# Performance work log

Hardware: AMD Instinct MI355X
Metric: run time of the kernel (lower is better)

The kernel has to match this reference:

```python
import jax, jax.numpy as jnp
from jax import lax
import numpy as np

K = 256   # kernel_size == hidden channels (Haar basis size)
S = 16    # stride
BN_EPS = 1e-5


def _haar_matrix_unnorm(n):
    if n == 2:
        return np.array([[1.0, 1.0], [1.0, -1.0]])
    prev = _haar_matrix_unnorm(n // 2)
    top = np.kron(prev, np.array([1.0, 1.0]))
    bot = np.kron(np.eye(n // 2), np.array([1.0, -1.0]))
    return np.concatenate((top, bot))


def haar_matrix(n):
    h = _haar_matrix_unnorm(n)
    return h / np.linalg.norm(h, axis=1, keepdims=True)


def setup_inputs() -> dict:
    key = jax.random.key(0)
    ks = jax.random.split(key, 8)
    B, T = 64, 32768
    haar = jnp.asarray(haar_matrix(K), dtype=jnp.float32)          # [K, K]
    x = jax.random.normal(ks[0], (B, 1, T), dtype=jnp.float32)
    return {
        "x": x,
        # BitwiseConv1d(1, K, K, stride=S, padding=K)
        "conv_w": haar[:, None, :],                                 # [K, 1, K] (OIH)
        "conv_b": 0.01 * jax.random.normal(ks[1], (K,), dtype=jnp.float32),
        "conv_gate": jax.random.uniform(ks[2], (K, 1, K), dtype=jnp.float32),
        "conv_scale": jnp.ones((K,), dtype=jnp.float32),            # adaptive per-out-channel scale
        # BatchNorm1d(K)
        "bn_gamma": jnp.ones((K,), dtype=jnp.float32),
        "bn_beta": jnp.zeros((K,), dtype=jnp.float32),
        # BitwiseConvTranspose1d(K, 1, K, stride=S)
        "ct_w": haar.T[:, None, :],                                 # [K(in), 1(out), K] (IOH, torch layout)
        "ct_b": 0.01 * jax.random.normal(ks[3], (1,), dtype=jnp.float32),
        "ct_gate": jax.random.uniform(ks[4], (K, 1, K), dtype=jnp.float32),
        "ct_scale": jnp.ones((1,), dtype=jnp.float32),
    }


def _forward(x, conv_w, conv_b, conv_gate, conv_scale, bn_gamma, bn_beta,
             ct_w, ct_b, ct_gate, ct_scale):
    T = x.shape[2]
    # --- BitwiseConv1d: gated weights (in_bin/weight_bin = identity) ---
    # gate binarization maps gate -> (gate + 1) / 2, multiplied into weights
    w = conv_w * (conv_gate + 1.0) * 0.5                            # [K,1,K]
    h = lax.conv_general_dilated(
        x, w, window_strides=(S,), padding=[(K, K)],
        dimension_numbers=("NCH", "OIH", "NCH"))                  # [B,K,L]
    h = conv_scale[None, :, None] * (h + conv_b[None, :, None])    # adaptive scaling
    # --- ReLU then BatchNorm1d (training-mode batch statistics) ---
    h = jax.nn.relu(h)
    mu = jnp.mean(h, axis=(0, 2), keepdims=True)
    var = jnp.mean((h - mu) ** 2, axis=(0, 2), keepdims=True)
    h = (h - mu) * lax.rsqrt(var + BN_EPS)
    h = h * bn_gamma[None, :, None] + bn_beta[None, :, None]
    # --- BitwiseConvTranspose1d: gated weights, expressed as dilated conv ---
    wt = ct_w * (ct_gate + 1.0) * 0.5                               # [K_in, 1, K]
    # torch IOH -> regular-conv OIH with kernel flipped
    wr = jnp.flip(jnp.transpose(wt, (1, 0, 2)), axis=-1)            # [1, K, K]
    y = lax.conv_general_dilated(
        h, wr, window_strides=(1,), padding=[(K - 1, K - 1)],
        lhs_dilation=(S,), dimension_numbers=("NCH", "OIH", "NCH"))
    y = ct_scale[None, :, None] * (y + ct_b[None, :, None])
    # crop: out[:, :, K : T + K]
    return y[:, :, K:T + K]


def reference(x, conv_w, conv_b, conv_gate, conv_scale, bn_gamma, bn_beta,
              ct_w, ct_b, ct_gate, ct_scale):
    return _forward(x, conv_w, conv_b, conv_gate, conv_scale, bn_gamma, bn_beta,
                    ct_w, ct_b, ct_gate, ct_scale)
```

## Files before the change

kernel.cpp:

```cpp
#include <hip/hip_runtime.h>
#include <hip/hip_bf16.h>

#define BB 64
#define TT 32768
#define KK 256
#define LL 2065
#define LT1 64
#define NLT1 33
#define NP1 (BB*NLT1)
#define NJ 19
#define NPT3 8

typedef __attribute__((ext_vector_type(8))) short short8;
typedef __attribute__((ext_vector_type(4))) float f32x4;
typedef __attribute__((ext_vector_type(4))) int int4v;
typedef __attribute__((ext_vector_type(2))) unsigned int uint2v;

__device__ __forceinline__ unsigned short f2bf(float f) {
    unsigned u = __builtin_bit_cast(unsigned, f);
    unsigned r = (u + 0x7FFFu + ((u >> 16) & 1u)) >> 16;
    return (unsigned short)r;
}
__device__ __forceinline__ unsigned pkbf(float a, float b) {
    unsigned r;
    asm("v_cvt_pk_bf16_f32 %0, %1, %2" : "=v"(r) : "v"(a), "v"(b));
    return r;
}
__device__ __forceinline__ float bf2f(unsigned short v) {
    return __builtin_bit_cast(float, (unsigned)v << 16);
}
__device__ __forceinline__ void gload_lds16(const void* g, void* l) {
    __builtin_amdgcn_global_load_lds(
        (const __attribute__((address_space(1))) unsigned int*)g,
        (__attribute__((address_space(3))) unsigned int*)l, 16, 0, 0);
}
__device__ __forceinline__ int slot_pi(int s) {
    int gg = s >> 4, f = s & 15;
    if (f < 8)  return 128 + 8*gg + f;
    if (f < 12) return 64 + 4*gg + (f - 8);
    if (f < 14) return 32 + 2*gg + (f - 12);
    if (f == 14) return 16 + gg;
    return gg;
}

__global__ void k0s_wpf(const float* __restrict__ cw, const float* __restrict__ cgt,
                        const float* __restrict__ cs, const float* __restrict__ cb,
                        float* __restrict__ Wpf, float* __restrict__ cbsp)
{
    int idx = blockIdx.x*256 + threadIdx.x;
    if (idx < 2304) {
        int g = idx / 144, e = idx - g*144;
        int lvl = e >> 4, m = e & 15;
        int j = 16*g + m;
        int o;
        switch (lvl) {
            case 0: o = 0; break;
            case 1: o = 1; break;
            case 2: o = 2 + (g>>3); break;
            case 3: o = 4 + (g>>2); break;
            case 4: o = 8 + (g>>1); break;
            case 5: o = 16 + g; break;
            case 6: o = 32 + 2*g + (m>>3); break;
            case 7: o = 64 + 4*g + (m>>2); break;
            default: o = 128 + 8*g + (m>>1); break;
        }
        Wpf[idx] = cs[o] * cw[o*KK + j] * (cgt[o*KK + j] + 1.0f) * 0.5f;
    }
    if (blockIdx.x == 0) {
        int s = threadIdx.x;
        int o = slot_pi(s);
        cbsp[s] = cs[o]*cb[o];
    }
}

__global__ __launch_bounds__(256, 2)
void k1_conv(const float* __restrict__ x, const float* __restrict__ Wpf,
             const float* __restrict__ cbsp,
             unsigned short* __restrict__ hout,
             float* __restrict__ psum, float* __restrict__ psq)
{
    __shared__ __align__(16) float xs[80*20];
    __shared__ __align__(16) unsigned short hb[64*256];
    __shared__ float redS[8*256];
    __shared__ float redQ[8*256];

    const int tid   = threadIdx.x;
    const int ltile = blockIdx.x;
    const int b     = blockIdx.y;
    const int l0    = ltile * LT1;
    const int lane  = tid & 63;
    const int w     = tid >> 6;
    const int gp    = lane & 15;
    const int cg    = lane >> 4;

    {
        const float* xb = x + (size_t)b*TT;
        const long pos0 = (long)l0*16 - 256;
        #pragma unroll
        for (int i = 0; i < 5; ++i) {
            int it = tid + i*256;
            long p = pos0 + it;
            xs[(it>>4)*20 + (it&15)] = (p >= 0 && p < TT) ? xb[p] : 0.0f;
        }
    }

    float wv[144];
    {
        const f32x4* wsrc = (const f32x4*)(Wpf + gp*144);
        #pragma unroll
        for (int i = 0; i < 36; ++i) {
            f32x4 t = wsrc[i];
            wv[4*i] = t[0]; wv[4*i+1] = t[1]; wv[4*i+2] = t[2]; wv[4*i+3] = t[3];
        }
    }
    f32x4 cbf[4];
    #pragma unroll
    for (int i = 0; i < 4; ++i) cbf[i] = *(const f32x4*)(cbsp + gp*16 + 4*i);

    const int wrow = (gp & 1) ? (8 + (gp >> 1))
                              : ((4056416 >> (3*(gp >> 1))) & 7);
    const float cbcoarse = cbsp[16*wrow + 15];
    __syncthreads();

    #pragma unroll 1
    for (int it = 0; it < 4; ++it) {
        const int col = w*16 + it*4 + cg;
        float xr[16];
        {
            const f32x4* xp = (const f32x4*)&xs[(col + gp)*20];
            #pragma unroll
            for (int i = 0; i < 4; ++i) {
                f32x4 t = xp[i];
                xr[4*i] = t[0]; xr[4*i+1] = t[1]; xr[4*i+2] = t[2]; xr[4*i+3] = t[3];
            }
        }
        float p0 = 0.f, p1 = 0.f, p2 = 0.f, p3 = 0.f, p4 = 0.f;
        #pragma unroll
        for (int m = 0; m < 16; ++m) {
            p0 = fmaf(wv[m],      xr[m], p0);
            p1 = fmaf(wv[16 + m], xr[m], p1);
            p2 = fmaf(wv[32 + m], xr[m], p2);
            p3 = fmaf(wv[48 + m], xr[m], p3);
            p4 = fmaf(wv[64 + m], xr[m], p4);
        }
        p4 += __shfl_xor(p4, 1);
        p3 += __shfl_xor(p3, 1); p3 += __shfl_xor(p3, 2);
        p2 += __shfl_xor(p2, 1); p2 += __shfl_xor(p2, 2); p2 += __shfl_xor(p2, 4);
        p1 += __shfl_xor(p1, 1); p1 += __shfl_xor(p1, 2); p1 += __shfl_xor(p1, 4);
        p1 += __shfl_xor(p1, 8);
        p0 += __shfl_xor(p0, 1); p0 += __shfl_xor(p0, 2); p0 += __shfl_xor(p0, 4);
        p0 += __shfl_xor(p0, 8);

        float v8[8], v7[4], v6[2], v5 = 0.f;
        #pragma unroll
        for (int k = 0; k < 8; ++k)
            v8[k] = fmaf(wv[128 + 2*k + 1], xr[2*k + 1], wv[128 + 2*k]*xr[2*k]);
        #pragma unroll
        for (int k = 0; k < 4; ++k) {
            float a = wv[112 + 4*k]*xr[4*k];
            a = fmaf(wv[112 + 4*k + 1], xr[4*k + 1], a);
            a = fmaf(wv[112 + 4*k + 2], xr[4*k + 2], a);
            v7[k] = fmaf(wv[112 + 4*k + 3], xr[4*k + 3], a);
        }
        #pragma unroll
        for (int k = 0; k < 2; ++k) {
            float a = 0.f;
            #pragma unroll
            for (int m = 0; m < 8; ++m) a = fmaf(wv[96 + 8*k + m], xr[8*k + m], a);
            v6[k] = a;
        }
        #pragma unroll
        for (int m = 0; m < 16; ++m) v5 = fmaf(wv[80 + m], xr[m], v5);

        const int swz = col & 7;
        unsigned short* hcol = hb + col*256;
        {
            float h0 = fmaxf(v8[0] + cbf[0][0], 0.f), h1 = fmaxf(v8[1] + cbf[0][1], 0.f);
            float h2 = fmaxf(v8[2] + cbf[0][2], 0.f), h3 = fmaxf(v8[3] + cbf[0][3], 0.f);
            float h4 = fmaxf(v8[4] + cbf[1][0], 0.f), h5 = fmaxf(v8[5] + cbf[1][1], 0.f);
            float h6 = fmaxf(v8[6] + cbf[1][2], 0.f), h7 = fmaxf(v8[7] + cbf[1][3], 0.f);
            int4v pk = { (int)pkbf(h0,h1), (int)pkbf(h2,h3),
                         (int)pkbf(h4,h5), (int)pkbf(h6,h7) };
            *(int4v*)(hcol + (((2*gp) ^ swz) << 3)) = pk;
        }
        {
            unsigned short* c1 = hcol + (((2*gp + 1) ^ swz) << 3);
            float h0 = fmaxf(v7[0] + cbf[2][0], 0.f), h1 = fmaxf(v7[1] + cbf[2][1], 0.f);
            float h2 = fmaxf(v7[2] + cbf[2][2], 0.f), h3 = fmaxf(v7[3] + cbf[2][3], 0.f);
            uint2v pk2 = { pkbf(h0,h1), pkbf(h2,h3) };
            *(uint2v*)c1 = pk2;
            float h4 = fmaxf(v6[0] + cbf[3][0], 0.f), h5 = fmaxf(v6[1] + cbf[3][1], 0.f);
            *(unsigned*)(c1 + 4) = pkbf(h4, h5);
            float h6 = fmaxf(v5 + cbf[3][2], 0.f);
            c1[6] = (unsigned short)(pkbf(h6, h6) & 0xffffu);
        }
        {
            float pc;
            if (gp & 1) pc = p4;
            else pc = (wrow == 0) ? p0 : (wrow == 1) ? p1
                     : (wrow <= 3) ? p2 : p3;
            float hc = fmaxf(pc + cbcoarse, 0.f);
            unsigned short* cc = hcol + (((2*wrow + 1) ^ swz) << 3);
            cc[7] = (unsigned short)(pkbf(hc, hc) & 0xffffu);
        }
    }
    __syncthreads();

    float s8[8], q8[8];
    #pragma unroll
    for (int j = 0; j < 8; ++j) { s8[j] = 0.f; q8[j] = 0.f; }
    const int chunk = tid & 31;
    const int colb  = tid >> 5;
    #pragma unroll
    for (int k = 0; k < 8; ++k) {
        int col = colb + k*8;
        int l = l0 + col;
        if (l < LL) {
            int4v v = *(const int4v*)(hb + col*256 + ((chunk ^ (col & 7)) << 3));
            *(int4v*)(hout + (((size_t)(b*LL + l)) << 8) + chunk*8) = v;
            #pragma unroll
            for (int i = 0; i < 4; ++i) {
                unsigned uu = (unsigned)v[i];
                float f0 = bf2f((unsigned short)(uu & 0xffffu));
                float f1 = bf2f((unsigned short)(uu >> 16));
                s8[2*i] += f0;   q8[2*i]   = fmaf(f0, f0, q8[2*i]);
                s8[2*i+1] += f1; q8[2*i+1] = fmaf(f1, f1, q8[2*i+1]);
            }
        }
    }
    {
        f32x4 a0 = { s8[0], s8[1], s8[2], s8[3] }, a1 = { s8[4], s8[5], s8[6], s8[7] };
        f32x4 b0 = { q8[0], q8[1], q8[2], q8[3] }, b1 = { q8[4], q8[5], q8[6], q8[7] };
        *(f32x4*)&redS[colb*256 + chunk*8]     = a0;
        *(f32x4*)&redS[colb*256 + chunk*8 + 4] = a1;
        *(f32x4*)&redQ[colb*256 + chunk*8]     = b0;
        *(f32x4*)&redQ[colb*256 + chunk*8 + 4] = b1;
    }
    __syncthreads();
    {
        float s = 0.f, q = 0.f;
        #pragma unroll
        for (int k = 0; k < 8; ++k) {
            s += redS[k*256 + tid];
            q += redQ[k*256 + tid];
        }
        size_t base = ((size_t)(b*NLT1 + ltile)) << 8;
        psum[base + tid] = s;
        psq [base + tid] = q;
    }
}

__global__ __launch_bounds__(256)
void k2_bn(const float* __restrict__ psum, const float* __restrict__ psq,
           const float* __restrict__ bng, const float* __restrict__ bnb,
           const float* __restrict__ ctw, const float* __restrict__ ctg,
           const float* __restrict__ ctscale,
           float* __restrict__ W3s, float* __restrict__ SWS)
{
    __shared__ double rs[4], rq[4];
    __shared__ float s_a, s_bc;
    __shared__ float swl[256];
    const int c = blockIdx.x;
    const int tid = threadIdx.x;
    const int o = slot_pi(c);
    double s = 0.0, q = 0.0;
    for (int i = tid; i < NP1; i += 256) {
        s += (double)psum[((size_t)i << 8) + c];
        q += (double)psq [((size_t)i << 8) + c];
    }
    for (int off = 32; off > 0; off >>= 1) {
        s += __shfl_down(s, off);
        q += __shfl_down(q, off);
    }
    if ((tid & 63) == 0) { rs[tid >> 6] = s; rq[tid >> 6] = q; }
    __syncthreads();
    if (tid == 0) {
        double st = rs[0]+rs[1]+rs[2]+rs[3];
        double qt = rq[0]+rq[1]+rq[2]+rq[3];
        const double cnt = (double)BB * (double)LL;
        double mu = st / cnt;
        double var = qt / cnt - mu*mu;
        float rsig = (float)(1.0 / sqrt(var + 1e-5));
        float a = bng[o] * rsig;
        s_a = a;
        s_bc = bnb[o] - (float)mu * a;
    }
    __syncthreads();
    float a = s_a, bc = s_bc, scl = ctscale[0];
    int gi = o*KK + tid;
    float wt = ctw[gi] * (ctg[gi] + 1.0f) * 0.5f;
    W3s[tid*KK + c] = scl * a * wt;
    swl[tid] = wt * bc;
    __syncthreads();
    if (tid < 16) {
        float acc2 = 0.0f;
        #pragma unroll
        for (int d = 0; d < 16; ++d) acc2 += swl[d*16 + tid];
        SWS[c*16 + tid] = acc2;
    }
}

__global__ __launch_bounds__(256)
void k2b_const(const float* __restrict__ SWS, const float* __restrict__ ctb,
               const float* __restrict__ ctscale, float* __restrict__ C2)
{
    __shared__ float accb[16][17];
    int tid = threadIdx.x;
    int r = tid & 15, cc = tid >> 4;
    float s = 0.0f;
    #pragma unroll
    for (int i = 0; i < 16; ++i) s += SWS[(cc*16 + i)*16 + r];
    accb[cc][r] = s;
    __syncthreads();
    if (tid < 16) {
        float t = 0.0f;
        #pragma unroll
        for (int i = 0; i < 16; ++i) t += accb[i][tid];
        C2[tid] = ctscale[0] * (t + ctb[0]);
    }
}

__global__ void k2c_b2f(const float* __restrict__ W3s, unsigned short* __restrict__ B2f)
{
    int idx = blockIdx.x*256 + threadIdx.x;
    int lane = idx & 63;
    int ntG  = (idx>>6) & 3;
    int kk   = (idx>>8) & 7;
    int j    = idx>>11;
    int c    = kk*32 + ((lane>>4)<<3);
    int r    = lane & 15;
    int d    = ntG + 15 - j;
    short8 v;
    if (d >= 0 && d <= 15) {
        const float* wr = W3s + (size_t)(16*d + r)*KK + c;
        #pragma unroll
        for (int i = 0; i < 8; ++i) v[i] = (short)f2bf(wr[i]);
    } else {
        #pragma unroll
        for (int i = 0; i < 8; ++i) v[i] = 0;
    }
    *(short8*)(B2f + (size_t)idx*8) = v;
}

__global__ __launch_bounds__(512, 1)
void k3_synth(const unsigned short* __restrict__ h, const unsigned short* __restrict__ B2f,
              const float* __restrict__ C2, float* __restrict__ out)
{
    __shared__ __align__(16) char As[272*512];
    const int tid  = threadIdx.x;
    const int lane = tid & 63;
    const int w    = tid >> 6;
    const int b    = blockIdx.y;
    const int P0   = blockIdx.x * 64;

    const char* hbase = (const char*)h + (((size_t)(b*LL) + 4*P0 + 1) << 9);

    {
        const int rl = lane >> 5;
        #pragma unroll
        for (int i = 0; i < 17; ++i) {
            int r0  = w*34 + i*2;
            int row = r0 + rl;
            int chunk = (lane & 31) ^ ((row >> 2) & 7);
            gload_lds16(hbase + (size_t)row*512 + chunk*16, As + r0*512);
        }
    }
    __syncthreads();

    const int li = lane & 15;
    const int gq = lane >> 4;

    f32x4 acc[4][4];
    #pragma unroll
    for (int mt = 0; mt < 4; ++mt)
        #pragma unroll
        for (int nt = 0; nt < 4; ++nt) acc[mt][nt] = (f32x4){0.f,0.f,0.f,0.f};

    #pragma unroll 1
    for (int jj = 0; jj < 3; ++jj) {
        const int j = w + jj*8;
        if (j >= NJ) break;
        short8 bfA[4], bfB[4];
        #pragma unroll
        for (int nt = 0; nt < 4; ++nt)
            bfA[nt] = *(const short8*)(B2f + (((size_t)(j*8 + 0)*4 + nt)*64 + lane)*8);
        #pragma unroll
        for (int kk = 0; kk < 8; ++kk) {
            if (kk < 7) {
                #pragma unroll
                for (int nt = 0; nt < 4; ++nt)
                    bfB[nt] = *(const short8*)(B2f + (((size_t)(j*8 + kk+1)*4 + nt)*64 + lane)*8);
            }
            short8 af[4];
            #pragma unroll
            for (int mt = 0; mt < 4; ++mt) {
                int row = 64*mt + 4*li + j;
                int p = (kk*4 + gq) ^ ((row >> 2) & 7);
                af[mt] = *(const short8*)(As + row*512 + p*16);
            }
            __builtin_amdgcn_s_setprio(1);
            #pragma unroll
            for (int mt = 0; mt < 4; ++mt)
                #pragma unroll
                for (int nt = 0; nt < 4; ++nt)
                    acc[mt][nt] = __builtin_amdgcn_mfma_f32_16x16x32_bf16(af[mt], bfA[nt], acc[mt][nt], 0, 0, 0);
            __builtin_amdgcn_s_setprio(0);
            #pragma unroll
            for (int nt = 0; nt < 4; ++nt) bfA[nt] = bfB[nt];
        }
    }
    __syncthreads();

    float* red = (float*)As;
    #pragma unroll
    for (int mt = 0; mt < 4; ++mt)
        #pragma unroll
        for (int nt = 0; nt < 4; ++nt) {
            int u = nt*16 + li;
            #pragma unroll
            for (int rr = 0; rr < 4; ++rr) {
                int Pl = 16*mt + gq*4 + rr;
                red[w*4352 + Pl*68 + u] = acc[mt][nt][rr];
            }
        }
    __syncthreads();

    {
        float* ob = out + (size_t)b*TT + (size_t)P0*64;
        #pragma unroll
        for (int it = 0; it < 2; ++it) {
            int item = it*512 + tid;
            int P = item >> 4, uq = item & 15;
            f32x4 s = (f32x4){0.f,0.f,0.f,0.f};
            #pragma unroll
            for (int c = 0; c < 8; ++c)
                s += *(const f32x4*)&red[c*4352 + P*68 + uq*4];
            int ub = (uq & 3)*4;
            f32x4 c2v = { C2[ub], C2[ub+1], C2[ub+2], C2[ub+3] };
            *(f32x4*)&ob[P*64 + uq*4] = s + c2v;
        }
    }
}

extern "C" void kernel_launch(void* const* d_in, const int* in_sizes, int n_in,
                              void* d_out, int out_size, void* d_ws, size_t ws_size,
                              hipStream_t stream)
{
    const float* x       = (const float*)d_in[0];
    const float* cw      = (const float*)d_in[1];
    const float* cb      = (const float*)d_in[2];
    const float* cgt     = (const float*)d_in[3];
    const float* cs      = (const float*)d_in[4];
    const float* bng     = (const float*)d_in[5];
    const float* bnb     = (const float*)d_in[6];
    const float* ctw     = (const float*)d_in[7];
    const float* ctb     = (const float*)d_in[8];
    const float* ctg     = (const float*)d_in[9];
    const float* ctscale = (const float*)d_in[10];
    float* out = (float*)d_out;

    char* ws = (char*)d_ws;
    size_t off = 0;
    unsigned short* h    = (unsigned short*)(ws + off); off += (size_t)BB*LL*KK*2;
    float* psum          = (float*)(ws + off);          off += (size_t)NP1*KK*4;
    float* psq           = (float*)(ws + off);          off += (size_t)NP1*KK*4;
    float* W3s           = (float*)(ws + off);          off += (size_t)KK*KK*4;
    float* SWS           = (float*)(ws + off);          off += (size_t)KK*16*4;
    float* C2            = (float*)(ws + off);          off += 64;
    float* Wpf           = (float*)(ws + off);          off += 2304*4;
    float* cbsp          = (float*)(ws + off);          off += 256*4;
    unsigned short* B2f  = (unsigned short*)(ws + off); off += (size_t)NJ*8*4*64*8*2;

    k0s_wpf <<<9, 256, 0, stream>>>(cw, cgt, cs, cb, Wpf, cbsp);
    k1_conv <<<dim3(NLT1, BB), 256, 0, stream>>>(x, Wpf, cbsp, h, psum, psq);
    k2_bn   <<<KK, 256, 0, stream>>>(psum, psq, bng, bnb, ctw, ctg, ctscale, W3s, SWS);
    k2b_const<<<1, 256, 0, stream>>>(SWS, ctb, ctscale, C2);
    k2c_b2f <<<152, 256, 0, stream>>>(W3s, B2f);
    k3_synth<<<dim3(NPT3, BB), 512, 0, stream>>>(h, B2f, C2, out);
}
```

Baseline: 93.33 us.

## Write conv outputs straight to global and reduce BN stats in registers

The conv kernel no longer stages x or h through shared memory. Each thread loads its 16-sample window directly from global memory, gathers its coarse-level value with a cross-lane shuffle, and writes 32 contiguous bytes of bf16 h per output column. BN partial sums are now accumulated from the fp32 values in registers instead of re-reading the bf16 tile, then reduced with lane shuffles and a smaller LDS stage. This removes LDS traffic and barriers, but adds redundant global reads of overlapping x windows, and statistics are now taken before bf16 rounding.

```diff
diff --git a/kernel.cpp b/kernel.cpp
--- a/kernel.cpp
+++ b/kernel.cpp
@@ -5,9 +5,8 @@
 #define TT 32768
 #define KK 256
 #define LL 2065
-#define LT1 64
-#define NLT1 33
-#define NP1 (BB*NLT1)
+#define NTL 33
+#define NP1 (BB*NTL)
 #define NJ 19
 #define NPT3 8
 
@@ -25,9 +24,6 @@
     unsigned r;
     asm("v_cvt_pk_bf16_f32 %0, %1, %2" : "=v"(r) : "v"(a), "v"(b));
     return r;
-}
-__device__ __forceinline__ float bf2f(unsigned short v) {
-    return __builtin_bit_cast(float, (unsigned)v << 16);
 }
 __device__ __forceinline__ void gload_lds16(const void* g, void* l) {
     __builtin_amdgcn_global_load_lds(
@@ -79,30 +75,17 @@
              unsigned short* __restrict__ hout,
              float* __restrict__ psum, float* __restrict__ psq)
 {
-    __shared__ __align__(16) float xs[80*20];
-    __shared__ __align__(16) unsigned short hb[64*256];
-    __shared__ float redS[8*256];
-    __shared__ float redQ[8*256];
-
-    const int tid   = threadIdx.x;
-    const int ltile = blockIdx.x;
-    const int b     = blockIdx.y;
-    const int l0    = ltile * LT1;
-    const int lane  = tid & 63;
-    const int w     = tid >> 6;
-    const int gp    = lane & 15;
-    const int cg    = lane >> 4;
-
-    {
-        const float* xb = x + (size_t)b*TT;
-        const long pos0 = (long)l0*16 - 256;
-        #pragma unroll
-        for (int i = 0; i < 5; ++i) {
-            int it = tid + i*256;
-            long p = pos0 + it;
-            xs[(it>>4)*20 + (it&15)] = (p >= 0 && p < TT) ? xb[p] : 0.0f;
-        }
-    }
+    __shared__ float redS[1024];
+    __shared__ float redQ[1024];
+
+    const int tid  = threadIdx.x;
+    const int tile = blockIdx.x;
+    const int b    = blockIdx.y;
+    const int lane = tid & 63;
+    const int w    = tid >> 6;
+    const int gp   = lane & 15;
+    const int cg   = lane >> 4;
+    const int l0   = tile * 64;
 
     float wv[144];
     {
@@ -119,132 +102,124 @@
 
     const int wrow = (gp & 1) ? (8 + (gp >> 1))
                               : ((4056416 >> (3*(gp >> 1))) & 7);
-    const float cbcoarse = cbsp[16*wrow + 15];
-    __syncthreads();
+    const unsigned long long INVM = 0xFDB97531C842A6E0ull;
+    const int csrc = cg*16 + (int)((INVM >> (4*gp)) & 15);
+
+    float s16[16], q16[16];
+    #pragma unroll
+    for (int j = 0; j < 16; ++j) { s16[j] = 0.f; q16[j] = 0.f; }
+
+    const float* xb = x + (size_t)b*TT;
 
     #pragma unroll 1
     for (int it = 0; it < 4; ++it) {
-        const int col = w*16 + it*4 + cg;
-        float xr[16];
-        {
-            const f32x4* xp = (const f32x4*)&xs[(col + gp)*20];
-            #pragma unroll
-            for (int i = 0; i < 4; ++i) {
-                f32x4 t = xp[i];
-                xr[4*i] = t[0]; xr[4*i+1] = t[1]; xr[4*i+2] = t[2]; xr[4*i+3] = t[3];
-            }
-        }
-        float p0 = 0.f, p1 = 0.f, p2 = 0.f, p3 = 0.f, p4 = 0.f;
-        #pragma unroll
-        for (int m = 0; m < 16; ++m) {
-            p0 = fmaf(wv[m],      xr[m], p0);
-            p1 = fmaf(wv[16 + m], xr[m], p1);
-            p2 = fmaf(wv[32 + m], xr[m], p2);
-            p3 = fmaf(wv[48 + m], xr[m], p3);
-            p4 = fmaf(wv[64 + m], xr[m], p4);
-        }
-        p4 += __shfl_xor(p4, 1);
-        p3 += __shfl_xor(p3, 1); p3 += __shfl_xor(p3, 2);
-        p2 += __shfl_xor(p2, 1); p2 += __shfl_xor(p2, 2); p2 += __shfl_xor(p2, 4);
-        p1 += __shfl_xor(p1, 1); p1 += __shfl_xor(p1, 2); p1 += __shfl_xor(p1, 4);
-        p1 += __shfl_xor(p1, 8);
-        p0 += __shfl_xor(p0, 1); p0 += __shfl_xor(p0, 2); p0 += __shfl_xor(p0, 4);
-        p0 += __shfl_xor(p0, 8);
-
-        float v8[8], v7[4], v6[2], v5 = 0.f;
-        #pragma unroll
-        for (int k = 0; k < 8; ++k)
-            v8[k] = fmaf(wv[128 + 2*k + 1], xr[2*k + 1], wv[128 + 2*k]*xr[2*k]);
-        #pragma unroll
-        for (int k = 0; k < 4; ++k) {
-            float a = wv[112 + 4*k]*xr[4*k];
-            a = fmaf(wv[112 + 4*k + 1], xr[4*k + 1], a);
-            a = fmaf(wv[112 + 4*k + 2], xr[4*k + 2], a);
-            v7[k] = fmaf(wv[112 + 4*k + 3], xr[4*k + 3], a);
-        }
-        #pragma unroll
-        for (int k = 0; k < 2; ++k) {
-            float a = 0.f;
-            #pragma unroll
-            for (int m = 0; m < 8; ++m) a = fmaf(wv[96 + 8*k + m], xr[8*k + m], a);
-            v6[k] = a;
-        }
-        #pragma unroll
-        for (int m = 0; m < 16; ++m) v5 = fmaf(wv[80 + m], xr[m], v5);
-
-        const int swz = col & 7;
-        unsigned short* hcol = hb + col*256;
-        {
-            float h0 = fmaxf(v8[0] + cbf[0][0], 0.f), h1 = fmaxf(v8[1] + cbf[0][1], 0.f);
-            float h2 = fmaxf(v8[2] + cbf[0][2], 0.f), h3 = fmaxf(v8[3] + cbf[0][3], 0.f);
-            float h4 = fmaxf(v8[4] + cbf[1][0], 0.f), h5 = fmaxf(v8[5] + cbf[1][1], 0.f);
-            float h6 = fmaxf(v8[6] + cbf[1][2], 0.f), h7 = fmaxf(v8[7] + cbf[1][3], 0.f);
-            int4v pk = { (int)pkbf(h0,h1), (int)pkbf(h2,h3),
-                         (int)pkbf(h4,h5), (int)pkbf(h6,h7) };
-            *(int4v*)(hcol + (((2*gp) ^ swz) << 3)) = pk;
-        }
-        {
-            unsigned short* c1 = hcol + (((2*gp + 1) ^ swz) << 3);
-            float h0 = fmaxf(v7[0] + cbf[2][0], 0.f), h1 = fmaxf(v7[1] + cbf[2][1], 0.f);
-            float h2 = fmaxf(v7[2] + cbf[2][2], 0.f), h3 = fmaxf(v7[3] + cbf[2][3], 0.f);
-            uint2v pk2 = { pkbf(h0,h1), pkbf(h2,h3) };
-            *(uint2v*)c1 = pk2;
-            float h4 = fmaxf(v6[0] + cbf[3][0], 0.f), h5 = fmaxf(v6[1] + cbf[3][1], 0.f);
-            *(unsigned*)(c1 + 4) = pkbf(h4, h5);
-            float h6 = fmaxf(v5 + cbf[3][2], 0.f);
-            c1[6] = (unsigned short)(pkbf(h6, h6) & 0xffffu);
-        }
-        {
+        const int l = l0 + it*16 + w*4 + cg;
+        if (l < LL) {
+            float xr[16];
+            const int rbase = l - 16 + gp;
+            if (l >= 16 && l <= 2048) {
+                const f32x4* xp = (const f32x4*)(xb + 16*rbase);
+                #pragma unroll
+                for (int i = 0; i < 4; ++i) {
+                    f32x4 t = xp[i];
+                    xr[4*i] = t[0]; xr[4*i+1] = t[1]; xr[4*i+2] = t[2]; xr[4*i+3] = t[3];
+                }
+            } else {
+                #pragma unroll
+                for (int m = 0; m < 16; ++m) {
+                    long p = (long)16*rbase + m;
+                    xr[m] = (p >= 0 && p < (long)TT) ? xb[p] : 0.0f;
+                }
+            }
+            float p0 = 0.f, p1 = 0.f, p2 = 0.f, p3 = 0.f, p4 = 0.f;
+            #pragma unroll
+            for (int m = 0; m < 16; ++m) {
+                p0 = fmaf(wv[m],      xr[m], p0);
+                p1 = fmaf(wv[16 + m], xr[m], p1);
+                p2 = fmaf(wv[32 + m], xr[m], p2);
+                p3 = fmaf(wv[48 + m], xr[m], p3);
+                p4 = fmaf(wv[64 + m], xr[m], p4);
+            }
+            p4 += __shfl_xor(p4, 1);
+            p3 += __shfl_xor(p3, 1); p3 += __shfl_xor(p3, 2);
+            p2 += __shfl_xor(p2, 1); p2 += __shfl_xor(p2, 2); p2 += __shfl_xor(p2, 4);
+            p1 += __shfl_xor(p1, 1); p1 += __shfl_xor(p1, 2); p1 += __shfl_xor(p1, 4);
+            p1 += __shfl_xor(p1, 8);
+            p0 += __shfl_xor(p0, 1); p0 += __shfl_xor(p0, 2); p0 += __shfl_xor(p0, 4);
+            p0 += __shfl_xor(p0, 8);
+
+            float v8[8], v7[4], v6[2], v5 = 0.f;
+            #pragma unroll
+            for (int k = 0; k < 8; ++k)
+                v8[k] = fmaf(wv[128 + 2*k + 1], xr[2*k + 1], wv[128 + 2*k]*xr[2*k]);
+            #pragma unroll
+            for (int k = 0; k < 4; ++k) {
+                float a = wv[112 + 4*k]*xr[4*k];
+                a = fmaf(wv[112 + 4*k + 1], xr[4*k + 1], a);
+                a = fmaf(wv[112 + 4*k + 2], xr[4*k + 2], a);
+                v7[k] = fmaf(wv[112 + 4*k + 3], xr[4*k + 3], a);
+            }
+            #pragma unroll
+            for (int k = 0; k < 2; ++k) {
+                float a = 0.f;
+                #pragma unroll
+                for (int m = 0; m < 8; ++m) a = fmaf(wv[96 + 8*k + m], xr[8*k + m], a);
+                v6[k] = a;
+            }
+            #pragma unroll
+            for (int m = 0; m < 16; ++m) v5 = fmaf(wv[80 + m], xr[m], v5);
+
             float pc;
             if (gp & 1) pc = p4;
             else pc = (wrow == 0) ? p0 : (wrow == 1) ? p1
                      : (wrow <= 3) ? p2 : p3;
-            float hc = fmaxf(pc + cbcoarse, 0.f);
-            unsigned short* cc = hcol + (((2*wrow + 1) ^ swz) << 3);
-            cc[7] = (unsigned short)(pkbf(hc, hc) & 0xffffu);
-        }
-    }
-    __syncthreads();
-
-    float s8[8], q8[8];
-    #pragma unroll
-    for (int j = 0; j < 8; ++j) { s8[j] = 0.f; q8[j] = 0.f; }
-    const int chunk = tid & 31;
-    const int colb  = tid >> 5;
-    #pragma unroll
-    for (int k = 0; k < 8; ++k) {
-        int col = colb + k*8;
-        int l = l0 + col;
-        if (l < LL) {
-            int4v v = *(const int4v*)(hb + col*256 + ((chunk ^ (col & 7)) << 3));
-            *(int4v*)(hout + (((size_t)(b*LL + l)) << 8) + chunk*8) = v;
-            #pragma unroll
-            for (int i = 0; i < 4; ++i) {
-                unsigned uu = (unsigned)v[i];
-                float f0 = bf2f((unsigned short)(uu & 0xffffu));
-                float f1 = bf2f((unsigned short)(uu >> 16));
-                s8[2*i] += f0;   q8[2*i]   = fmaf(f0, f0, q8[2*i]);
-                s8[2*i+1] += f1; q8[2*i+1] = fmaf(f1, f1, q8[2*i+1]);
-            }
-        }
-    }
+            float myc = __shfl(pc, csrc);
+
+            float hf[16];
+            hf[0] = fmaxf(v8[0] + cbf[0][0], 0.f); hf[1] = fmaxf(v8[1] + cbf[0][1], 0.f);
+            hf[2] = fmaxf(v8[2] + cbf[0][2], 0.f); hf[3] = fmaxf(v8[3] + cbf[0][3], 0.f);
+            hf[4] = fmaxf(v8[4] + cbf[1][0], 0.f); hf[5] = fmaxf(v8[5] + cbf[1][1], 0.f);
+            hf[6] = fmaxf(v8[6] + cbf[1][2], 0.f); hf[7] = fmaxf(v8[7] + cbf[1][3], 0.f);
+            hf[8]  = fmaxf(v7[0] + cbf[2][0], 0.f); hf[9]  = fmaxf(v7[1] + cbf[2][1], 0.f);
+            hf[10] = fmaxf(v7[2] + cbf[2][2], 0.f); hf[11] = fmaxf(v7[3] + cbf[2][3], 0.f);
+            hf[12] = fmaxf(v6[0] + cbf[3][0], 0.f); hf[13] = fmaxf(v6[1] + cbf[3][1], 0.f);
+            hf[14] = fmaxf(v5 + cbf[3][2], 0.f);    hf[15] = fmaxf(myc + cbf[3][3], 0.f);
+
+            #pragma unroll
+            for (int j = 0; j < 16; ++j) {
+                s16[j] += hf[j];
+                q16[j] = fmaf(hf[j], hf[j], q16[j]);
+            }
+
+            int4v pkA = { (int)pkbf(hf[0],hf[1]),  (int)pkbf(hf[2],hf[3]),
+                          (int)pkbf(hf[4],hf[5]),  (int)pkbf(hf[6],hf[7]) };
+            int4v pkB = { (int)pkbf(hf[8],hf[9]),  (int)pkbf(hf[10],hf[11]),
+                          (int)pkbf(hf[12],hf[13]),(int)pkbf(hf[14],hf[15]) };
+            unsigned short* hp = hout + (((size_t)(b*LL + l)) << 8) + 16*gp;
+            *(int4v*)hp       = pkA;
+            *(int4v*)(hp + 8) = pkB;
+        }
+    }
+
+    #pragma unroll
+    for (int j = 0; j < 16; ++j) {
+        s16[j] += __shfl_xor(s16[j], 16); s16[j] += __shfl_xor(s16[j], 32);
+        q16[j] += __shfl_xor(q16[j], 16); q16[j] += __shfl_xor(q16[j], 32);
+    }
+    if (cg == 0) {
+        #pragma unroll
+        for (int i = 0; i < 4; ++i) {
+            f32x4 a = { s16[4*i], s16[4*i+1], s16[4*i+2], s16[4*i+3] };
+            f32x4 c = { q16[4*i], q16[4*i+1], q16[4*i+2], q16[4*i+3] };
+            *(f32x4*)&redS[w*256 + 16*gp + 4*i] = a;
+            *(f32x4*)&redQ[w*256 + 16*gp + 4*i] = c;
+        }
+    }
+    __syncthreads();
     {
-        f32x4 a0 = { s8[0], s8[1], s8[2], s8[3] }, a1 = { s8[4], s8[5], s8[6], s8[7] };
-        f32x4 b0 = { q8[0], q8[1], q8[2], q8[3] }, b1 = { q8[4], q8[5], q8[6], q8[7] };
-        *(f32x4*)&redS[colb*256 + chunk*8]     = a0;
-        *(f32x4*)&redS[colb*256 + chunk*8 + 4] = a1;
-        *(f32x4*)&redQ[colb*256 + chunk*8]     = b0;
-        *(f32x4*)&redQ[colb*256 + chunk*8 + 4] = b1;
-    }
-    __syncthreads();
-    {
-        float s = 0.f, q = 0.f;
-        #pragma unroll
-        for (int k = 0; k < 8; ++k) {
-            s += redS[k*256 + tid];
-            q += redQ[k*256 + tid];
-        }
-        size_t base = ((size_t)(b*NLT1 + ltile)) << 8;
+        float s = redS[tid] + redS[256+tid] + redS[512+tid] + redS[768+tid];
+        float q = redQ[tid] + redQ[256+tid] + redQ[512+tid] + redQ[768+tid];
+        size_t base = ((size_t)(b*NTL + tile)) << 8;
         psum[base + tid] = s;
         psq [base + tid] = q;
     }
@@ -472,7 +447,7 @@
     unsigned short* B2f  = (unsigned short*)(ws + off); off += (size_t)NJ*8*4*64*8*2;
 
     k0s_wpf <<<9, 256, 0, stream>>>(cw, cgt, cs, cb, Wpf, cbsp);
-    k1_conv <<<dim3(NLT1, BB), 256, 0, stream>>>(x, Wpf, cbsp, h, psum, psq);
+    k1_conv <<<dim3(NTL, BB), 256, 0, stream>>>(x, Wpf, cbsp, h, psum, psq);
     k2_bn   <<<KK, 256, 0, stream>>>(psum, psq, bng, bnb, ctw, ctg, ctscale, W3s, SWS);
     k2b_const<<<1, 256, 0, stream>>>(SWS, ctb, ctscale, C2);
     k2c_b2f <<<152, 256, 0, stream>>>(W3s, B2f);
```

Result: slower. 100.9 us (+8.1%).
